# Optimization experiments

Measured on AMD Instinct MI355X. Metric: run time of the kernel, lower is better.

## Reference

```python
import jax, jax.numpy as jnp
import numpy as np

B, S, E, NH = 2, 2048, 1024, 8
DH = E // NH


def setup_inputs() -> dict:
    key = jax.random.key(0)
    ks = jax.random.split(key, 8)
    q = jax.random.normal(ks[0], (B, S, E), dtype=jnp.float32)
    k = jax.random.normal(ks[1], (B, S, E), dtype=jnp.float32)
    v = jax.random.normal(ks[2], (B, S, E), dtype=jnp.float32)
    # gate projections: Linear(3E -> NH)
    igate_w = jax.random.normal(ks[3], (NH, 3 * E), dtype=jnp.float32) * 0.02
    igate_b = jax.random.normal(ks[4], (NH,), dtype=jnp.float32) * 0.1
    fgate_w = jax.random.normal(ks[5], (NH, 3 * E), dtype=jnp.float32) * 0.02
    fgate_b = jnp.linspace(3.0, 6.0, NH, dtype=jnp.float32)  # bias_linspace_init_
    norm_weight = 1.0 + 0.01 * jax.random.normal(ks[6], (E,), dtype=jnp.float32)
    return {"q": q, "k": k, "v": v, "igate_w": igate_w, "igate_b": igate_b,
            "fgate_w": fgate_w, "fgate_b": fgate_b, "norm_weight": norm_weight}


def _mlstm_forward(q, k, v, igate_w, igate_b, fgate_w, fgate_b, norm_weight):
    eps = 1e-6
    gate_in = jnp.concatenate([q, k, v], axis=-1)            # (B,S,3E)
    i_pre = gate_in @ igate_w.T + igate_b                    # (B,S,NH)
    f_pre = gate_in @ fgate_w.T + fgate_b                    # (B,S,NH)
    i_pre = jnp.transpose(i_pre, (0, 2, 1))                  # (B,NH,S)
    f_pre = jnp.transpose(f_pre, (0, 2, 1))                  # (B,NH,S)

    qh = jnp.transpose(q.reshape(B, S, NH, DH), (0, 2, 1, 3))  # (B,NH,S,DH)
    kh = jnp.transpose(k.reshape(B, S, NH, DH), (0, 2, 1, 3))
    vh = jnp.transpose(v.reshape(B, S, NH, DH), (0, 2, 1, 3))

    # cumulative log forget gates; decay matrix D[i,j] = sum_{u=j+1..i} logsig(f_u) + i_pre[j]
    log_fg = jax.nn.log_sigmoid(f_pre)                       # (B,NH,S)
    cs = jnp.cumsum(log_fg, axis=-1)                         # (B,NH,S)
    diff = cs[:, :, :, None] - cs[:, :, None, :]             # (B,NH,S,S) = cs[i]-cs[j]
    causal = jnp.tril(jnp.ones((S, S), dtype=bool))
    log_fg_mat = jnp.where(causal, diff, -jnp.inf)
    log_D = log_fg_mat + i_pre[:, :, None, :]                # (B,NH,S,S)

    max_log_D = jnp.max(log_D, axis=-1, keepdims=True)       # rowwise stabilizer
    D = jnp.exp(log_D - max_log_D)

    qk = jnp.einsum("bhsd,bhtd->bhst", qh, kh / jnp.sqrt(jnp.float32(DH)))
    C = qk * D
    normalizer = jnp.maximum(jnp.abs(jnp.sum(C, axis=-1, keepdims=True)),
                             jnp.exp(-max_log_D))
    Cn = C / (normalizer + eps)
    h = jnp.einsum("bhst,bhtd->bhsd", Cn, vh)                # (B,NH,S,DH)

    # MultiHeadLayerNorm == group_norm(num_groups=NH): per-head, per-token over DH
    mu = jnp.mean(h, axis=-1, keepdims=True)
    var = jnp.var(h, axis=-1, keepdims=True)
    hn = (h - mu) / jnp.sqrt(var + 1e-5)
    hn = hn * norm_weight.reshape(NH, DH)[None, :, None, :]
    return jnp.transpose(hn, (0, 2, 1, 3)).reshape(B, S, E)


def reference(q, k, v, igate_w, igate_b, fgate_w, fgate_b, norm_weight):
    return _mlstm_forward(q, k, v, igate_w, igate_b, fgate_w, fgate_b, norm_weight)
```

## Files before the change

kernel.cpp:

```cpp
#include <hip/hip_runtime.h>
#include <hip/hip_bf16.h>
#include <math.h>

typedef __attribute__((ext_vector_type(8))) short bf16x8;
typedef __attribute__((ext_vector_type(4))) float f32x4;

namespace {
constexpr int kB = 2, kS = 2048, kE = 1024, kNH = 8, kDH = 128, kE3 = 3072;
constexpr float kLog2e = 1.4426950408889634f;
constexpr int BM = 64, BN = 64;
}

__device__ __forceinline__ ushort f2bf(float x) {
  union { __hip_bfloat16 b; ushort u; } c; c.b = __float2bfloat16(x); return c.u;
}
__device__ __forceinline__ uint pk2(float a, float b) {
  return (uint)f2bf(a) | ((uint)f2bf(b) << 16);
}
__device__ __forceinline__ void gload16(const void* g, void* l) {
  __builtin_amdgcn_global_load_lds(
      (const __attribute__((address_space(1))) void*)g,
      (__attribute__((address_space(3))) void*)l, 16, 0, 0);
}

__device__ __forceinline__ float butterfly64(float* acc, int lane) {
  int cur = 64;
#pragma unroll
  for (int lv = 0; lv < 6; ++lv) {
    const int bmask = 1 << lv;
    const int half = cur >> 1;
    const bool hi = (lane & bmask) != 0;
#pragma unroll
    for (int i = 0; i < 32; ++i) {
      if (i >= half) break;
      const float keep = hi ? acc[i + half] : acc[i];
      const float send = hi ? acc[i] : acc[i + half];
      acc[i] = keep + __shfl_xor(send, bmask);
    }
    cur = half;
  }
  return acc[0];
}

__global__ __launch_bounds__(256, 1) void preproc_kernel(
    const float* __restrict__ q, const float* __restrict__ k, const float* __restrict__ v,
    const float* __restrict__ iw, const float* __restrict__ ib,
    const float* __restrict__ fw, const float* __restrict__ fb,
    ushort* __restrict__ Kb, ushort* __restrict__ Vtb,
    float* __restrict__ i_pre, float* __restrict__ f_pre) {
  const int b = blockIdx.y;
  const int s0 = blockIdx.x * 16;
  const int tid = threadIdx.x;
  const int w = tid >> 6, lane = tid & 63;
  __shared__ ushort Vst[16 * 1024];

#pragma unroll
  for (int t = 0; t < 4; ++t) {
    const int tokl = w * 4 + t;
    const int s = s0 + tokl;
    const size_t base = ((size_t)b * kS + s) * kE + lane * 16;
    const float4 k0 = *reinterpret_cast<const float4*>(k + base);
    const float4 k1 = *reinterpret_cast<const float4*>(k + base + 4);
    const float4 k2 = *reinterpret_cast<const float4*>(k + base + 8);
    const float4 k3 = *reinterpret_cast<const float4*>(k + base + 12);
    uint4 pa, pb;
    pa.x = pk2(k0.x, k0.y); pa.y = pk2(k0.z, k0.w);
    pa.z = pk2(k1.x, k1.y); pa.w = pk2(k1.z, k1.w);
    pb.x = pk2(k2.x, k2.y); pb.y = pk2(k2.z, k2.w);
    pb.z = pk2(k3.x, k3.y); pb.w = pk2(k3.z, k3.w);
    ushort* kd = Kb + ((size_t)(b * 8 + (lane >> 3)) * kS + s) * 128 + (lane & 7) * 16;
    *reinterpret_cast<uint4*>(kd) = pa;
    *reinterpret_cast<uint4*>(kd + 8) = pb;

    const float4 v0 = *reinterpret_cast<const float4*>(v + base);
    const float4 v1 = *reinterpret_cast<const float4*>(v + base + 4);
    const float4 v2 = *reinterpret_cast<const float4*>(v + base + 8);
    const float4 v3 = *reinterpret_cast<const float4*>(v + base + 12);
    uint4 va, vb4;
    va.x = pk2(v0.x, v0.y); va.y = pk2(v0.z, v0.w);
    va.z = pk2(v1.x, v1.y); va.w = pk2(v1.z, v1.w);
    vb4.x = pk2(v2.x, v2.y); vb4.y = pk2(v2.z, v2.w);
    vb4.z = pk2(v3.x, v3.y); vb4.w = pk2(v3.z, v3.w);
    const int cc0 = lane * 2, cc1 = lane * 2 + 1;
    *reinterpret_cast<uint4*>(reinterpret_cast<char*>(Vst) + tokl * 2048 +
                              ((cc0 ^ ((cc0 >> 3) & 7)) << 4)) = va;
    *reinterpret_cast<uint4*>(reinterpret_cast<char*>(Vst) + tokl * 2048 +
                              ((cc1 ^ ((cc1 >> 3) & 7)) << 4)) = vb4;
  }
  __syncthreads();

#pragma unroll
  for (int j = 0; j < 4; ++j) {
    const int e = j * 256 + tid;
    const int cc = e >> 3;
    const int off = ((cc ^ ((cc >> 3) & 7)) << 4) + (e & 7) * 2;
    uint tmp[8];
#pragma unroll
    for (int t2 = 0; t2 < 16; t2 += 2) {
      const ushort u0 = *reinterpret_cast<const ushort*>(
          reinterpret_cast<const char*>(Vst) + t2 * 2048 + off);
      const ushort u1 = *reinterpret_cast<const ushort*>(
          reinterpret_cast<const char*>(Vst) + (t2 + 1) * 2048 + off);
      tmp[t2 >> 1] = (uint)u0 | ((uint)u1 << 16);
    }
    uint4 o0, o1;
    o0.x = tmp[0]; o0.y = tmp[1]; o0.z = tmp[2]; o0.w = tmp[3];
    o1.x = tmp[4]; o1.y = tmp[5]; o1.z = tmp[6]; o1.w = tmp[7];
    ushort* vd = Vtb + ((size_t)(b * 8 + (e >> 7)) * 128 + (e & 127)) * kS + s0;
    *reinterpret_cast<uint4*>(vd) = o0;
    *reinterpret_cast<uint4*>(vd + 8) = o1;
  }

  float* red = reinterpret_cast<float*>(Vst);
  for (int tg = 0; tg < 2; ++tg) {
    float acc[128];
#pragma unroll
    for (int i = 0; i < 128; ++i) acc[i] = 0.f;
    for (int step = 0; step < 12; ++step) {
      const int ebase = w * 768 + step * 64;
      const int seg = ebase >> 10;
      const int eo = (ebase & 1023) + lane;
      const int e = ebase + lane;
      const float* __restrict__ src = (seg == 0) ? q : (seg == 1) ? k : v;
      float gv[8];
#pragma unroll
      for (int t = 0; t < 8; ++t)
        gv[t] = src[((size_t)b * kS + s0 + tg * 8 + t) * kE + eo];
      float wi[8], wf[8];
#pragma unroll
      for (int h = 0; h < 8; ++h) {
        wi[h] = iw[h * kE3 + e];
        wf[h] = fw[h * kE3 + e];
      }
#pragma unroll
      for (int t = 0; t < 8; ++t) {
#pragma unroll
        for (int h = 0; h < 8; ++h) {
          acc[t * 16 + h]     += gv[t] * wi[h];
          acc[t * 16 + 8 + h] += gv[t] * wf[h];
        }
      }
    }
    const float r0 = butterfly64(acc, lane);
    const float r1 = butterfly64(acc + 64, lane);
    const int a = ((lane & 1) << 5) | ((lane & 2) << 3) | ((lane & 4) << 1) |
                  ((lane & 8) >> 1) | ((lane & 16) >> 3) | ((lane & 32) >> 5);
    __syncthreads();
    red[w * 128 + a] = r0;
    red[w * 128 + 64 + a] = r1;
    __syncthreads();
    if (tid < 128) {
      const float val = red[tid] + red[128 + tid] + red[256 + tid] + red[384 + tid];
      const int tok_lo = tid >> 4, gate = tid & 15, h = gate & 7;
      const int token = s0 + tg * 8 + tok_lo;
      const size_t idx = ((size_t)(b * 8 + h)) * kS + token;
      if (gate < 8) i_pre[idx] = val + ib[h];
      else          f_pre[idx] = val + fb[h];
    }
  }
}

__global__ __launch_bounds__(256) void scan_kernel(
    const float* __restrict__ i_pre, const float* __restrict__ f_pre,
    float* __restrict__ a2_out, float* __restrict__ M2_out, float* __restrict__ nfl_out) {
  const int bh = blockIdx.x;
  const int tid = threadIdx.x;
  const int w = tid >> 6, lane = tid & 63;
  __shared__ float wsum[4], wmax[4];
  const float* __restrict__ fp = f_pre + (size_t)bh * kS;
  const float* __restrict__ ip = i_pre + (size_t)bh * kS;
  const int s0 = tid * 8;

  const float4 fa = *reinterpret_cast<const float4*>(fp + s0);
  const float4 fb4 = *reinterpret_cast<const float4*>(fp + s0 + 4);
  float lf[8];
  {
    const float fv[8] = {fa.x, fa.y, fa.z, fa.w, fb4.x, fb4.y, fb4.z, fb4.w};
#pragma unroll
    for (int j = 0; j < 8; ++j)
      lf[j] = fminf(fv[j], 0.f) - log1pf(expf(-fabsf(fv[j])));
  }
  float run = 0.f, pcs[8];
#pragma unroll
  for (int j = 0; j < 8; ++j) { run += lf[j]; pcs[j] = run; }
  float x = run;
#pragma unroll
  for (int d = 1; d < 64; d <<= 1) {
    const float t = __shfl_up(x, d);
    if (lane >= d) x += t;
  }
  if (lane == 63) wsum[w] = x;
  __syncthreads();
  float woff = 0.f;
#pragma unroll
  for (int i = 0; i < 4; ++i) if (i < w) woff += wsum[i];
  const float csbase = woff + x - run;
  float cs[8];
#pragma unroll
  for (int j = 0; j < 8; ++j) cs[j] = csbase + pcs[j];

  const float4 ia = *reinterpret_cast<const float4*>(ip + s0);
  const float4 ib4 = *reinterpret_cast<const float4*>(ip + s0 + 4);
  float av[8];
  {
    const float iv[8] = {ia.x, ia.y, ia.z, ia.w, ib4.x, ib4.y, ib4.z, ib4.w};
#pragma unroll
    for (int j = 0; j < 8; ++j) av[j] = iv[j] - cs[j];
  }
  float rmax = -1e30f, pm[8];
#pragma unroll
  for (int j = 0; j < 8; ++j) { rmax = fmaxf(rmax, av[j]); pm[j] = rmax; }
  float mi = rmax;
#pragma unroll
  for (int d = 1; d < 64; d <<= 1) {
    const float t = __shfl_up(mi, d);
    if (lane >= d) mi = fmaxf(mi, t);
  }
  if (lane == 63) wmax[w] = mi;
  float mexcl = __shfl_up(mi, 1);
  if (lane == 0) mexcl = -1e30f;
  __syncthreads();
  float wmoff = -1e30f;
#pragma unroll
  for (int i = 0; i < 4; ++i) if (i < w) wmoff = fmaxf(wmoff, wmax[i]);
  const float mbase = fmaxf(wmoff, mexcl);

  float4 a2lo, a2hi, m2lo, m2hi, nflo, nfhi;
  float M[8];
#pragma unroll
  for (int j = 0; j < 8; ++j) M[j] = fmaxf(mbase, pm[j]);
  a2lo.x = av[0] * kLog2e; a2lo.y = av[1] * kLog2e; a2lo.z = av[2] * kLog2e; a2lo.w = av[3] * kLog2e;
  a2hi.x = av[4] * kLog2e; a2hi.y = av[5] * kLog2e; a2hi.z = av[6] * kLog2e; a2hi.w = av[7] * kLog2e;
  m2lo.x = M[0] * kLog2e; m2lo.y = M[1] * kLog2e; m2lo.z = M[2] * kLog2e; m2lo.w = M[3] * kLog2e;
  m2hi.x = M[4] * kLog2e; m2hi.y = M[5] * kLog2e; m2hi.z = M[6] * kLog2e; m2hi.w = M[7] * kLog2e;
  nflo.x = expf(-(cs[0] + M[0])); nflo.y = expf(-(cs[1] + M[1]));
  nflo.z = expf(-(cs[2] + M[2])); nflo.w = expf(-(cs[3] + M[3]));
  nfhi.x = expf(-(cs[4] + M[4])); nfhi.y = expf(-(cs[5] + M[5]));
  nfhi.z = expf(-(cs[6] + M[6])); nfhi.w = expf(-(cs[7] + M[7]));
  const size_t o = (size_t)bh * kS + s0;
  *reinterpret_cast<float4*>(a2_out + o) = a2lo;
  *reinterpret_cast<float4*>(a2_out + o + 4) = a2hi;
  *reinterpret_cast<float4*>(M2_out + o) = m2lo;
  *reinterpret_cast<float4*>(M2_out + o + 4) = m2hi;
  *reinterpret_cast<float4*>(nfl_out + o) = nflo;
  *reinterpret_cast<float4*>(nfl_out + o + 4) = nfhi;
}

__global__ __launch_bounds__(256, 2) void attn_mfma_kernel(
    const float* __restrict__ qg, const ushort* __restrict__ Kb,
    const ushort* __restrict__ Vtb,
    const float* __restrict__ a2, const float* __restrict__ M2,
    const float* __restrict__ nfl, const float* __restrict__ nw,
    float* __restrict__ out) {
  const int bh = blockIdx.y;
  const int b = bh >> 3, h = bh & 7;
  const int it = (int)gridDim.x - 1 - (int)blockIdx.x;
  const int tid = threadIdx.x;
  const int w = tid >> 6, lane = tid & 63;
  const int l15 = lane & 15, g = lane >> 4;
  const int row0 = it * BM;
  const int rowbase = row0 + w * 16;
  const size_t bhS = (size_t)bh * kS;

  __shared__ ushort Klds[2 * BN * kDH];
  __shared__ ushort Vlds[2 * kDH * BN];
  __shared__ ushort Plds[4][16 * BN];

  const char* __restrict__ KgBase = reinterpret_cast<const char*>(Kb + bhS * 128);
  const char* __restrict__ VgBase = reinterpret_cast<const char*>(Vtb + (size_t)bh * 128 * kS);

  bf16x8 qf[4];
  {
    const float scale = 0.08838834764831845f;
    const float* qrow = qg + ((size_t)b * kS + rowbase + l15) * kE + h * kDH;
#pragma unroll
    for (int ks = 0; ks < 4; ++ks) {
      const float4 lo = *reinterpret_cast<const float4*>(qrow + ks * 32 + g * 8);
      const float4 hi = *reinterpret_cast<const float4*>(qrow + ks * 32 + g * 8 + 4);
      bf16x8 f;
      f[0] = (short)f2bf(lo.x * scale); f[1] = (short)f2bf(lo.y * scale);
      f[2] = (short)f2bf(lo.z * scale); f[3] = (short)f2bf(lo.w * scale);
      f[4] = (short)f2bf(hi.x * scale); f[5] = (short)f2bf(hi.y * scale);
      f[6] = (short)f2bf(hi.z * scale); f[7] = (short)f2bf(hi.w * scale);
      qf[ks] = f;
    }
  }
  float M2row[4];
#pragma unroll
  for (int reg = 0; reg < 4; ++reg) M2row[reg] = M2[bhS + rowbase + g * 4 + reg];

  int koffG[4], voffG[4];
#pragma unroll
  for (int i = 0; i < 4; ++i) {
    const int L = tid * 16 + i * 4096;
    { const int j = L >> 8, c = (L >> 4) & 15;
      koffG[i] = j * 256 + ((c ^ (j & 7)) << 4); }
    { const int d = L >> 7, c = (L >> 4) & 7;
      voffG[i] = d * 4096 + ((c ^ (d & 7)) << 4); }
  }

  auto stage = [&](int buf, int jt) {
    const char* Kg = KgBase + (size_t)jt * 16384;
    const char* Vg = VgBase + (size_t)jt * 128;
    char* kl = reinterpret_cast<char*>(Klds) + buf * 16384 + tid * 16;
    char* vl = reinterpret_cast<char*>(Vlds) + buf * 16384 + tid * 16;
#pragma unroll
    for (int i = 0; i < 4; ++i) gload16(Kg + koffG[i], kl + i * 4096);
#pragma unroll
    for (int i = 0; i < 4; ++i) gload16(Vg + voffG[i], vl + i * 4096);
  };

  f32x4 hacc[8];
#pragma unroll
  for (int db = 0; db < 8; ++db) hacc[db] = (f32x4){0.f, 0.f, 0.f, 0.f};
  float rs[4] = {0.f, 0.f, 0.f, 0.f};

  float avc[4];
#pragma unroll
  for (int cb = 0; cb < 4; ++cb) avc[cb] = a2[bhS + cb * 16 + l15];
  stage(0, 0);
  __syncthreads();

  for (int jt = 0; jt <= it; ++jt) {
    const int cur = jt & 1;
    float avn[4];
    if (jt < it) {
      stage(cur ^ 1, jt + 1);
#pragma unroll
      for (int cb = 0; cb < 4; ++cb)
        avn[cb] = a2[bhS + (jt + 1) * 64 + cb * 16 + l15];
    }

    const int kbase = cur * 16384;
    f32x4 sacc[4];
#pragma unroll
    for (int cb = 0; cb < 4; ++cb) sacc[cb] = (f32x4){0.f, 0.f, 0.f, 0.f};
#pragma unroll
    for (int ks = 0; ks < 4; ++ks) {
#pragma unroll
      for (int cb = 0; cb < 4; ++cb) {
        const int j = cb * 16 + l15;
        const int kb = kbase + j * 256 + ((ks * 64 + g * 16) ^ ((l15 & 7) << 4));
        const bf16x8 kf = *reinterpret_cast<const bf16x8*>(
            reinterpret_cast<const char*>(Klds) + kb);
        sacc[cb] = __builtin_amdgcn_mfma_f32_16x16x32_bf16(qf[ks], kf, sacc[cb], 0, 0, 0);
      }
    }

#pragma unroll
    for (int cb = 0; cb < 4; ++cb) {
      const int jg = jt * 64 + cb * 16 + l15;
#pragma unroll
      for (int reg = 0; reg < 4; ++reg) {
        const int ig = rowbase + g * 4 + reg;
        float val = 0.f;
        if (jg <= ig) val = sacc[cb][reg] * exp2f(avc[cb] - M2row[reg]);
        rs[reg] += val;
        const int r = g * 4 + reg;
        const int pb = r * 128 + ((cb * 32 + l15 * 2) ^ ((r & 7) << 4));
        *reinterpret_cast<ushort*>(
            reinterpret_cast<char*>(&Plds[w][0]) + pb) = f2bf(val);
      }
    }

    const int vbase = cur * 16384;
#pragma unroll
    for (int ks2 = 0; ks2 < 2; ++ks2) {
      const int pbyte = l15 * 128 + ((ks2 * 64 + g * 16) ^ ((l15 & 7) << 4));
      const bf16x8 pf = *reinterpret_cast<const bf16x8*>(
          reinterpret_cast<const char*>(&Plds[w][0]) + pbyte);
#pragma unroll
      for (int db = 0; db < 8; ++db) {
        const int d = db * 16 + l15;
        const int vb = vbase + d * 128 + ((ks2 * 64 + g * 16) ^ ((d & 7) << 4));
        const bf16x8 vf = *reinterpret_cast<const bf16x8*>(
            reinterpret_cast<const char*>(Vlds) + vb);
        hacc[db] = __builtin_amdgcn_mfma_f32_16x16x32_bf16(vf, pf, hacc[db], 0, 0, 0);
      }
    }
    __syncthreads();
    if (jt < it) {
#pragma unroll
      for (int cb = 0; cb < 4; ++cb) avc[cb] = avn[cb];
    }
  }

#pragma unroll
  for (int reg = 0; reg < 4; ++reg) {
    float x = rs[reg];
    x += __shfl_xor(x, 1); x += __shfl_xor(x, 2);
    x += __shfl_xor(x, 4); x += __shfl_xor(x, 8);
    rs[reg] = x;
  }
  float* rsp = reinterpret_cast<float*>(&Plds[w][0]);
  if (l15 == 0) {
#pragma unroll
    for (int reg = 0; reg < 4; ++reg) rsp[g * 4 + reg] = rs[reg];
  }
  const float rsum = rsp[l15];
  const float nf = nfl[bhS + rowbase + l15];
  const float inv = 1.f / (fmaxf(fabsf(rsum), nf) + 1e-6f);
  float ps = 0.f, pq = 0.f;
#pragma unroll
  for (int db = 0; db < 8; ++db) {
#pragma unroll
    for (int reg = 0; reg < 4; ++reg) {
      const float hv = hacc[db][reg] * inv;
      hacc[db][reg] = hv;
      ps += hv; pq += hv * hv;
    }
  }
  ps += __shfl_xor(ps, 16); ps += __shfl_xor(ps, 32);
  pq += __shfl_xor(pq, 16); pq += __shfl_xor(pq, 32);
  const float mu = ps * (1.f / 128.f);
  const float var = pq * (1.f / 128.f) - mu * mu;
  const float rstd = rsqrtf(var + 1e-5f);
  const int srow = rowbase + l15;
  float* __restrict__ orow = out + ((size_t)b * kS + srow) * kE + h * kDH;
#pragma unroll
  for (int db = 0; db < 8; ++db) {
    const int d0 = db * 16 + g * 4;
    const float4 nw4 = *reinterpret_cast<const float4*>(nw + h * kDH + d0);
    float4 o;
    o.x = (hacc[db][0] - mu) * rstd * nw4.x;
    o.y = (hacc[db][1] - mu) * rstd * nw4.y;
    o.z = (hacc[db][2] - mu) * rstd * nw4.z;
    o.w = (hacc[db][3] - mu) * rstd * nw4.w;
    *reinterpret_cast<float4*>(orow + d0) = o;
  }
}

extern "C" void kernel_launch(void* const* d_in, const int* in_sizes, int n_in,
                              void* d_out, int out_size, void* d_ws, size_t ws_size,
                              hipStream_t stream) {
  const float* q  = (const float*)d_in[0];
  const float* k  = (const float*)d_in[1];
  const float* v  = (const float*)d_in[2];
  const float* iw = (const float*)d_in[3];
  const float* ib = (const float*)d_in[4];
  const float* fw = (const float*)d_in[5];
  const float* fb = (const float*)d_in[6];
  const float* nw = (const float*)d_in[7];
  float* out = (float*)d_out;

  char* ws = (char*)d_ws;
  const int BHS = kB * kNH * kS;
  float* i_pre = (float*)ws;
  float* f_pre = i_pre + BHS;
  float* a2    = i_pre + 2 * BHS;
  float* M2    = i_pre + 3 * BHS;
  float* nfl   = i_pre + 4 * BHS;
  char* ws2 = ws + (size_t)5 * BHS * 4;
  ushort* Kb  = (ushort*)ws2;
  ushort* Vtb = Kb + (size_t)kB * kNH * kS * kDH;

  preproc_kernel<<<dim3(kS / 16, kB), dim3(256), 0, stream>>>(
      q, k, v, iw, ib, fw, fb, Kb, Vtb, i_pre, f_pre);
  scan_kernel<<<dim3(kB * kNH), dim3(256), 0, stream>>>(i_pre, f_pre, a2, M2, nfl);
  attn_mfma_kernel<<<dim3(kS / BM, kB * kNH), dim3(256), 0, stream>>>(
      q, Kb, Vtb, a2, M2, nfl, nw, out);
}
```

Measured before the change: 123.8 us.

## Split long causal attention rows across two blocks and add combine kernel

Query tiles 16..31 of the causal attention are now split into two key-range chunks. Each chunk writes partial unnormalized h and row sums to workspace, and a new combine kernel sums them and applies the normalization and layernorm. This balances per-block work and raises the block count from 32 to 48 per head. Separately, the fused preprocessing kernel is split into a K/V bf16 conversion kernel with smaller tiles and a gates kernel that spreads the i/f projections across warps. The cost is two extra launches and extra global traffic for the partial results.

```diff
diff --git a/kernel.cpp b/kernel.cpp
--- a/kernel.cpp
+++ b/kernel.cpp
@@ -9,6 +9,8 @@
 constexpr int kB = 2, kS = 2048, kE = 1024, kNH = 8, kDH = 128, kE3 = 3072;
 constexpr float kLog2e = 1.4426950408889634f;
 constexpr int BM = 64, BN = 64;
+constexpr int kHeavy = 16;
+constexpr int kUnits = 16 + 2 * 16;
 }
 
 __device__ __forceinline__ ushort f2bf(float x) {
@@ -42,21 +44,18 @@
   return acc[0];
 }
 
-__global__ __launch_bounds__(256, 1) void preproc_kernel(
-    const float* __restrict__ q, const float* __restrict__ k, const float* __restrict__ v,
-    const float* __restrict__ iw, const float* __restrict__ ib,
-    const float* __restrict__ fw, const float* __restrict__ fb,
-    ushort* __restrict__ Kb, ushort* __restrict__ Vtb,
-    float* __restrict__ i_pre, float* __restrict__ f_pre) {
+__global__ __launch_bounds__(256) void convkv_kernel(
+    const float* __restrict__ k, const float* __restrict__ v,
+    ushort* __restrict__ Kb, ushort* __restrict__ Vtb) {
   const int b = blockIdx.y;
-  const int s0 = blockIdx.x * 16;
+  const int s0 = blockIdx.x * 8;
   const int tid = threadIdx.x;
   const int w = tid >> 6, lane = tid & 63;
-  __shared__ ushort Vst[16 * 1024];
-
-#pragma unroll
-  for (int t = 0; t < 4; ++t) {
-    const int tokl = w * 4 + t;
+  __shared__ ushort Vst[8 * 1024];
+
+#pragma unroll
+  for (int t = 0; t < 2; ++t) {
+    const int tokl = w * 2 + t;
     const int s = s0 + tokl;
     const size_t base = ((size_t)b * kS + s) * kE + lane * 16;
     const float4 k0 = *reinterpret_cast<const float4*>(k + base);
@@ -94,69 +93,69 @@
     const int e = j * 256 + tid;
     const int cc = e >> 3;
     const int off = ((cc ^ ((cc >> 3) & 7)) << 4) + (e & 7) * 2;
-    uint tmp[8];
-#pragma unroll
-    for (int t2 = 0; t2 < 16; t2 += 2) {
+    uint tmp[4];
+#pragma unroll
+    for (int t2 = 0; t2 < 8; t2 += 2) {
       const ushort u0 = *reinterpret_cast<const ushort*>(
           reinterpret_cast<const char*>(Vst) + t2 * 2048 + off);
       const ushort u1 = *reinterpret_cast<const ushort*>(
           reinterpret_cast<const char*>(Vst) + (t2 + 1) * 2048 + off);
       tmp[t2 >> 1] = (uint)u0 | ((uint)u1 << 16);
     }
-    uint4 o0, o1;
-    o0.x = tmp[0]; o0.y = tmp[1]; o0.z = tmp[2]; o0.w = tmp[3];
-    o1.x = tmp[4]; o1.y = tmp[5]; o1.z = tmp[6]; o1.w = tmp[7];
+    uint4 o; o.x = tmp[0]; o.y = tmp[1]; o.z = tmp[2]; o.w = tmp[3];
     ushort* vd = Vtb + ((size_t)(b * 8 + (e >> 7)) * 128 + (e & 127)) * kS + s0;
-    *reinterpret_cast<uint4*>(vd) = o0;
-    *reinterpret_cast<uint4*>(vd + 8) = o1;
-  }
-
-  float* red = reinterpret_cast<float*>(Vst);
-  for (int tg = 0; tg < 2; ++tg) {
-    float acc[128];
-#pragma unroll
-    for (int i = 0; i < 128; ++i) acc[i] = 0.f;
-    for (int step = 0; step < 12; ++step) {
-      const int ebase = w * 768 + step * 64;
-      const int seg = ebase >> 10;
-      const int eo = (ebase & 1023) + lane;
-      const int e = ebase + lane;
-      const float* __restrict__ src = (seg == 0) ? q : (seg == 1) ? k : v;
-      float gv[8];
-#pragma unroll
-      for (int t = 0; t < 8; ++t)
-        gv[t] = src[((size_t)b * kS + s0 + tg * 8 + t) * kE + eo];
-      float wi[8], wf[8];
-#pragma unroll
-      for (int h = 0; h < 8; ++h) {
-        wi[h] = iw[h * kE3 + e];
-        wf[h] = fw[h * kE3 + e];
-      }
-#pragma unroll
-      for (int t = 0; t < 8; ++t) {
-#pragma unroll
-        for (int h = 0; h < 8; ++h) {
-          acc[t * 16 + h]     += gv[t] * wi[h];
-          acc[t * 16 + 8 + h] += gv[t] * wf[h];
-        }
-      }
-    }
-    const float r0 = butterfly64(acc, lane);
-    const float r1 = butterfly64(acc + 64, lane);
-    const int a = ((lane & 1) << 5) | ((lane & 2) << 3) | ((lane & 4) << 1) |
-                  ((lane & 8) >> 1) | ((lane & 16) >> 3) | ((lane & 32) >> 5);
-    __syncthreads();
-    red[w * 128 + a] = r0;
-    red[w * 128 + 64 + a] = r1;
-    __syncthreads();
-    if (tid < 128) {
-      const float val = red[tid] + red[128 + tid] + red[256 + tid] + red[384 + tid];
-      const int tok_lo = tid >> 4, gate = tid & 15, h = gate & 7;
-      const int token = s0 + tg * 8 + tok_lo;
-      const size_t idx = ((size_t)(b * 8 + h)) * kS + token;
-      if (gate < 8) i_pre[idx] = val + ib[h];
-      else          f_pre[idx] = val + fb[h];
-    }
+    *reinterpret_cast<uint4*>(vd) = o;
+  }
+}
+
+__global__ __launch_bounds__(256) void gates_kernel(
+    const float* __restrict__ q, const float* __restrict__ k, const float* __restrict__ v,
+    const float* __restrict__ iw, const float* __restrict__ ib,
+    const float* __restrict__ fw, const float* __restrict__ fb,
+    float* __restrict__ i_pre, float* __restrict__ f_pre) {
+  const int tid = threadIdx.x;
+  const int w = tid >> 6, lane = tid & 63;
+  const int tokbase = blockIdx.x * 8;
+  const int kh = w >> 1, gh = w & 1;
+  const float* __restrict__ W = gh ? fw : iw;
+
+  float acc[64];
+#pragma unroll
+  for (int i = 0; i < 64; ++i) acc[i] = 0.f;
+
+  for (int step = 0; step < 24; ++step) {
+    const int e = kh * 1536 + step * 64 + lane;
+    const int seg = e >> 10;
+    const int eo = e & 1023;
+    const float* __restrict__ src = (seg == 0) ? q : (seg == 1) ? k : v;
+    float gv[8];
+#pragma unroll
+    for (int t = 0; t < 8; ++t)
+      gv[t] = src[(size_t)(tokbase + t) * kE + eo];
+    float w8[8];
+#pragma unroll
+    for (int hh = 0; hh < 8; ++hh) w8[hh] = W[hh * kE3 + e];
+#pragma unroll
+    for (int t = 0; t < 8; ++t)
+#pragma unroll
+      for (int hh = 0; hh < 8; ++hh)
+        acc[t * 8 + hh] += gv[t] * w8[hh];
+  }
+  const float r = butterfly64(acc, lane);
+  const int a = ((lane & 1) << 5) | ((lane & 2) << 3) | ((lane & 4) << 1) |
+                ((lane & 8) >> 1) | ((lane & 16) >> 3) | ((lane & 32) >> 5);
+  __shared__ float red[4][64];
+  red[w][a] = r;
+  __syncthreads();
+  if (tid < 128) {
+    const int t = tid >> 4, g16 = tid & 15, hh = g16 & 7;
+    const float val = (g16 < 8) ? red[0][t * 8 + hh] + red[2][t * 8 + hh]
+                                : red[1][t * 8 + hh] + red[3][t * 8 + hh];
+    const int token = tokbase + t;
+    const int b = token >> 11, s = token & 2047;
+    const size_t idx = ((size_t)(b * 8 + hh)) * kS + s;
+    if (g16 < 8) i_pre[idx] = val + ib[hh];
+    else         f_pre[idx] = val + fb[hh];
   }
 }
 
@@ -225,10 +224,10 @@
   for (int i = 0; i < 4; ++i) if (i < w) wmoff = fmaxf(wmoff, wmax[i]);
   const float mbase = fmaxf(wmoff, mexcl);
 
+  float M[8];
+#pragma unroll
+  for (int j = 0; j < 8; ++j) M[j] = fmaxf(mbase, pm[j]);
   float4 a2lo, a2hi, m2lo, m2hi, nflo, nfhi;
-  float M[8];
-#pragma unroll
-  for (int j = 0; j < 8; ++j) M[j] = fmaxf(mbase, pm[j]);
   a2lo.x = av[0] * kLog2e; a2lo.y = av[1] * kLog2e; a2lo.z = av[2] * kLog2e; a2lo.w = av[3] * kLog2e;
   a2hi.x = av[4] * kLog2e; a2hi.y = av[5] * kLog2e; a2hi.z = av[6] * kLog2e; a2hi.w = av[7] * kLog2e;
   m2lo.x = M[0] * kLog2e; m2lo.y = M[1] * kLog2e; m2lo.z = M[2] * kLog2e; m2lo.w = M[3] * kLog2e;
@@ -246,15 +245,57 @@
   *reinterpret_cast<float4*>(nfl_out + o + 4) = nfhi;
 }
 
+__device__ __forceinline__ void epilogue_store(
+    f32x4* hacc, float rsum, float nf, int b, int h, int srow, int g,
+    const float* __restrict__ nw, float* __restrict__ out) {
+  const float inv = 1.f / (fmaxf(fabsf(rsum), nf) + 1e-6f);
+  float ps = 0.f, pq = 0.f;
+#pragma unroll
+  for (int db = 0; db < 8; ++db) {
+#pragma unroll
+    for (int reg = 0; reg < 4; ++reg) {
+      const float hv = hacc[db][reg] * inv;
+      hacc[db][reg] = hv;
+      ps += hv; pq += hv * hv;
+    }
+  }
+  ps += __shfl_xor(ps, 16); ps += __shfl_xor(ps, 32);
+  pq += __shfl_xor(pq, 16); pq += __shfl_xor(pq, 32);
+  const float mu = ps * (1.f / 128.f);
+  const float var = pq * (1.f / 128.f) - mu * mu;
+  const float rstd = rsqrtf(var + 1e-5f);
+  float* __restrict__ orow = out + ((size_t)b * kS + srow) * kE + h * kDH;
+#pragma unroll
+  for (int db = 0; db < 8; ++db) {
+    const int d0 = db * 16 + g * 4;
+    const float4 nw4 = *reinterpret_cast<const float4*>(nw + h * kDH + d0);
+    float4 o;
+    o.x = (hacc[db][0] - mu) * rstd * nw4.x;
+    o.y = (hacc[db][1] - mu) * rstd * nw4.y;
+    o.z = (hacc[db][2] - mu) * rstd * nw4.z;
+    o.w = (hacc[db][3] - mu) * rstd * nw4.w;
+    *reinterpret_cast<float4*>(orow + d0) = o;
+  }
+}
+
 __global__ __launch_bounds__(256, 2) void attn_mfma_kernel(
     const float* __restrict__ qg, const ushort* __restrict__ Kb,
     const ushort* __restrict__ Vtb,
     const float* __restrict__ a2, const float* __restrict__ M2,
     const float* __restrict__ nfl, const float* __restrict__ nw,
-    float* __restrict__ out) {
+    float* __restrict__ out, float* __restrict__ ph, float* __restrict__ prs) {
   const int bh = blockIdx.y;
   const int b = bh >> 3, h = bh & 7;
-  const int it = (int)gridDim.x - 1 - (int)blockIdx.x;
+  const int u = kUnits - 1 - (int)blockIdx.x;
+  int it, j0, j1, chunk = -1;
+  if (u < kHeavy) { it = u; j0 = 0; j1 = it; }
+  else {
+    const int t = (u - kHeavy) >> 1, c = (u - kHeavy) & 1;
+    it = kHeavy + t;
+    const int m = (it + 1) >> 1;
+    if (c == 0) { j0 = 0; j1 = m - 1; } else { j0 = m; j1 = it; }
+    chunk = ((bh * 16) + t) * 2 + c;
+  }
   const int tid = threadIdx.x;
   const int w = tid >> 6, lane = tid & 63;
   const int l15 = lane & 15, g = lane >> 4;
@@ -317,14 +358,14 @@
 
   float avc[4];
 #pragma unroll
-  for (int cb = 0; cb < 4; ++cb) avc[cb] = a2[bhS + cb * 16 + l15];
-  stage(0, 0);
+  for (int cb = 0; cb < 4; ++cb) avc[cb] = a2[bhS + j0 * 64 + cb * 16 + l15];
+  stage(0, j0);
   __syncthreads();
 
-  for (int jt = 0; jt <= it; ++jt) {
-    const int cur = jt & 1;
+  for (int jt = j0; jt <= j1; ++jt) {
+    const int cur = (jt - j0) & 1;
     float avn[4];
-    if (jt < it) {
+    if (jt < j1) {
       stage(cur ^ 1, jt + 1);
 #pragma unroll
       for (int cb = 0; cb < 4; ++cb)
@@ -379,7 +420,7 @@
       }
     }
     __syncthreads();
-    if (jt < it) {
+    if (jt < j1) {
 #pragma unroll
       for (int cb = 0; cb < 4; ++cb) avc[cb] = avn[cb];
     }
@@ -392,6 +433,21 @@
     x += __shfl_xor(x, 4); x += __shfl_xor(x, 8);
     rs[reg] = x;
   }
+
+  if (chunk >= 0) {
+    float* pdst = ph + (size_t)chunk * (BM * kDH) + tid * 32;
+#pragma unroll
+    for (int db = 0; db < 8; ++db)
+      *reinterpret_cast<float4*>(pdst + db * 4) =
+          make_float4(hacc[db][0], hacc[db][1], hacc[db][2], hacc[db][3]);
+    if (l15 == 0) {
+#pragma unroll
+      for (int reg = 0; reg < 4; ++reg)
+        prs[chunk * BM + w * 16 + g * 4 + reg] = rs[reg];
+    }
+    return;
+  }
+
   float* rsp = reinterpret_cast<float*>(&Plds[w][0]);
   if (l15 == 0) {
 #pragma unroll
@@ -399,35 +455,35 @@
   }
   const float rsum = rsp[l15];
   const float nf = nfl[bhS + rowbase + l15];
-  const float inv = 1.f / (fmaxf(fabsf(rsum), nf) + 1e-6f);
-  float ps = 0.f, pq = 0.f;
+  epilogue_store(hacc, rsum, nf, b, h, rowbase + l15, g, nw, out);
+}
+
+__global__ __launch_bounds__(256) void combine_kernel(
+    const float* __restrict__ ph, const float* __restrict__ prs,
+    const float* __restrict__ nfl, const float* __restrict__ nw,
+    float* __restrict__ out) {
+  const int blk = blockIdx.x;
+  const int bh = blk >> 4, t = blk & 15;
+  const int b = bh >> 3, h = bh & 7;
+  const int it = kHeavy + t;
+  const int tid = threadIdx.x;
+  const int w = tid >> 6, lane = tid & 63;
+  const int l15 = lane & 15, g = lane >> 4;
+  const int rowbase = it * BM + w * 16;
+  const int c0 = blk * 2, c1 = blk * 2 + 1;
+
+  f32x4 hacc[8];
+  const float* p0 = ph + (size_t)c0 * (BM * kDH) + tid * 32;
+  const float* p1 = ph + (size_t)c1 * (BM * kDH) + tid * 32;
 #pragma unroll
   for (int db = 0; db < 8; ++db) {
-#pragma unroll
-    for (int reg = 0; reg < 4; ++reg) {
-      const float hv = hacc[db][reg] * inv;
-      hacc[db][reg] = hv;
-      ps += hv; pq += hv * hv;
-    }
-  }
-  ps += __shfl_xor(ps, 16); ps += __shfl_xor(ps, 32);
-  pq += __shfl_xor(pq, 16); pq += __shfl_xor(pq, 32);
-  const float mu = ps * (1.f / 128.f);
-  const float var = pq * (1.f / 128.f) - mu * mu;
-  const float rstd = rsqrtf(var + 1e-5f);
-  const int srow = rowbase + l15;
-  float* __restrict__ orow = out + ((size_t)b * kS + srow) * kE + h * kDH;
-#pragma unroll
-  for (int db = 0; db < 8; ++db) {
-    const int d0 = db * 16 + g * 4;
-    const float4 nw4 = *reinterpret_cast<const float4*>(nw + h * kDH + d0);
-    float4 o;
-    o.x = (hacc[db][0] - mu) * rstd * nw4.x;
-    o.y = (hacc[db][1] - mu) * rstd * nw4.y;
-    o.z = (hacc[db][2] - mu) * rstd * nw4.z;
-    o.w = (hacc[db][3] - mu) * rstd * nw4.w;
-    *reinterpret_cast<float4*>(orow + d0) = o;
-  }
+    const float4 a = *reinterpret_cast<const float4*>(p0 + db * 4);
+    const float4 c = *reinterpret_cast<const float4*>(p1 + db * 4);
+    hacc[db] = (f32x4){a.x + c.x, a.y + c.y, a.z + c.z, a.w + c.w};
+  }
+  const float rsum = prs[c0 * BM + w * 16 + l15] + prs[c1 * BM + w * 16 + l15];
+  const float nf = nfl[(size_t)bh * kS + rowbase + l15];
+  epilogue_store(hacc, rsum, nf, b, h, rowbase + l15, g, nw, out);
 }
 
 extern "C" void kernel_launch(void* const* d_in, const int* in_sizes, int n_in,
@@ -453,10 +509,14 @@
   char* ws2 = ws + (size_t)5 * BHS * 4;
   ushort* Kb  = (ushort*)ws2;
   ushort* Vtb = Kb + (size_t)kB * kNH * kS * kDH;
-
-  preproc_kernel<<<dim3(kS / 16, kB), dim3(256), 0, stream>>>(
-      q, k, v, iw, ib, fw, fb, Kb, Vtb, i_pre, f_pre);
+  float* ph   = (float*)(Vtb + (size_t)kB * kNH * kS * kDH);
+  float* prs  = ph + (size_t)512 * BM * kDH;
+
+  convkv_kernel<<<dim3(kS / 8, kB), dim3(256), 0, stream>>>(k, v, Kb, Vtb);
+  gates_kernel<<<dim3(kB * kS / 8), dim3(256), 0, stream>>>(q, k, v, iw, ib, fw, fb,
+                                                            i_pre, f_pre);
   scan_kernel<<<dim3(kB * kNH), dim3(256), 0, stream>>>(i_pre, f_pre, a2, M2, nfl);
-  attn_mfma_kernel<<<dim3(kS / BM, kB * kNH), dim3(256), 0, stream>>>(
-      q, Kb, Vtb, a2, M2, nfl, nw, out);
-}
+  attn_mfma_kernel<<<dim3(kUnits, kB * kNH), dim3(256), 0, stream>>>(
+      q, Kb, Vtb, a2, M2, nfl, nw, out, ph, prs);
+  combine_kernel<<<dim3(kB * kNH * 16), dim3(256), 0, stream>>>(ph, prs, nfl, nw, out);
+}
```

New measurement: 122.4 us. About the same (-1.1%).
